# Performance work log

Measured on AMD Instinct MI355X. Metric: run time of the kernel, lower is better.

## Reference

```python
import jax, jax.numpy as jnp
import numpy as np

E, H, D = 512, 8, 64
B, T = 2, 1024
HD = H * D


def _linear(x, W, b):
    return x @ W + b


def _ln(x, g, b):
    mu = x.mean(-1, keepdims=True)
    var = ((x - mu) ** 2).mean(-1, keepdims=True)
    return (x - mu) / jnp.sqrt(var + 1e-5) * g + b


def _l2norm(x):
    n = jnp.sqrt((x * x).sum(-1, keepdims=True))
    return x / jnp.maximum(n, 1e-12)


def setup_inputs() -> dict:
    key = jax.random.key(0)
    ks = jax.random.split(key, 32)
    s = 0.02
    inp = {
        'x': jax.random.normal(ks[0], (B, T, E), jnp.float32),
        'b_min': jax.random.normal(ks[1], (B, T, E), jnp.float32),
        'b_max': jax.random.normal(ks[2], (B, T, E), jnp.float32),
        'motif_context': jax.random.normal(ks[3], (B, T, E), jnp.float32),
        'Wk': jax.random.normal(ks[4], (E, HD), jnp.float32) * s,
        'bk': jnp.zeros((HD,), jnp.float32),
        'Wq': jax.random.normal(ks[5], (E, HD), jnp.float32) * s,
        'bq': jnp.zeros((HD,), jnp.float32),
        'Wv': jax.random.normal(ks[6], (E, HD), jnp.float32) * s,
        'bv': jnp.zeros((HD,), jnp.float32),
        'Wo': jax.random.normal(ks[7], (HD, E), jnp.float32) * s,
        'bo': jnp.zeros((E,), jnp.float32),
        'Wd': jax.random.normal(ks[8], (E, H), jnp.float32) * s,
        'bd': jnp.zeros((H,), jnp.float32),
        'Wgw': jax.random.normal(ks[9], (E, H), jnp.float32) * s,
        'bgw': jnp.zeros((H,), jnp.float32),
        'Wgf': jax.random.normal(ks[10], (E, H), jnp.float32) * s,
        'bgf': jnp.zeros((H,), jnp.float32),
        'Wps': jax.random.normal(ks[11], (E, E), jnp.float32) * s,
        'bps': jnp.zeros((E,), jnp.float32),
        'ln1_g': jnp.ones((E,), jnp.float32),
        'ln1_b': jnp.zeros((E,), jnp.float32),
        'ln2_g': jnp.ones((E,), jnp.float32),
        'ln2_b': jnp.zeros((E,), jnp.float32),
        'W1': jax.random.normal(ks[12], (E, 4 * E), jnp.float32) * s,
        'b1': jnp.zeros((4 * E,), jnp.float32),
        'W2': jax.random.normal(ks[13], (4 * E, E), jnp.float32) * s,
        'b2': jnp.zeros((E,), jnp.float32),
    }
    return inp


def reference(x, b_min, b_max, motif_context,
              Wk, bk, Wq, bq, Wv, bv, Wo, bo, Wd, bd,
              Wgw, bgw, Wgf, bgf, Wps, bps,
              ln1_g, ln1_b, ln2_g, ln2_b, W1, b1, W2, b2):
    Bs, Ts, Es = x.shape
    x_n = _ln(x, ln1_g, ln1_b)
    k = _l2norm(_linear(x_n, Wk, bk).reshape(Bs, Ts, H, D))
    q = _l2norm(_linear(x_n, Wq, bq).reshape(Bs, Ts, H, D))
    v = jnp.tanh(_linear(x_n, Wv, bv).reshape(Bs, Ts, H, D))
    d = jax.nn.softplus(_linear(x_n, Wd, bd))            # (B,T,H)
    gw = jax.nn.sigmoid(_linear(x_n, Wgw, bgw)) ** 2     # (B,T,H)
    gf = 1.0 - jax.nn.sigmoid(_linear(x_n, Wgf, bgf)) ** 2

    # gated linear recurrent scan via cumsum of rank-1 updates
    v_gated = v * (d * gw)[..., None]                    # (B,T,H,D)
    updates = jnp.einsum('bthi,bthj->bthij', v_gated, k)  # (B,T,H,D,D)
    decay = jnp.clip(d * gf, 1e-6, 0.999)
    log_decay = jnp.log(decay)[..., None, None]          # (B,T,H,1,1)
    exp_cum_decay = jnp.exp(jnp.cumsum(log_decay, axis=1))
    state = jnp.cumsum(updates / (exp_cum_decay + 1e-8), axis=1) * exp_cum_decay
    readout = jnp.einsum('bthij,bthj->bthi', state, q)   # (B,T,H,D)
    next_mem = state[:, -1]

    x2 = x + _linear(readout.reshape(Bs, Ts, HD), Wo, bo) + 0.1 * motif_context
    h = _ln(x2, ln2_g, ln2_b)
    x3 = x2 + _linear(jax.nn.gelu(_linear(h, W1, b1), approximate=False), W2, b2)
    probe = _linear(x3, Wps, bps)
    return (x3, next_mem, b_min + probe, b_max + probe)
```

## Files before the change

### kernel.cpp

```cpp
#include <hip/hip_runtime.h>


typedef unsigned short u16;
typedef unsigned int u32;
typedef __attribute__((ext_vector_type(8))) short short8;
typedef __attribute__((ext_vector_type(4))) float floatx4;

__device__ __forceinline__ float b2f(u16 u) {
  u32 x = ((u32)u) << 16;
  return __uint_as_float(x);
}
__device__ __forceinline__ u16 f2b(float f) {
  u32 x = __float_as_uint(f);
  u32 r = (x + 0x7fffu + ((x >> 16) & 1u)) >> 16;
  return (u16)r;
}
__device__ __forceinline__ float4 b4_to_f4(uint2 u) {
  float4 r;
  r.x = __uint_as_float((u.x & 0xffffu) << 16);
  r.y = __uint_as_float(u.x & 0xffff0000u);
  r.z = __uint_as_float((u.y & 0xffffu) << 16);
  r.w = __uint_as_float(u.y & 0xffff0000u);
  return r;
}

__device__ __forceinline__ void stage16(const u16* g, u16* lds_wave_base) {
  __builtin_amdgcn_global_load_lds((const __attribute__((address_space(1))) void*)g,
                                   (__attribute__((address_space(3))) void*)lds_wave_base,
                                   16, 0, 0);
}

template <int ROWS>
__device__ __forceinline__ void stage_tile64(const u16* __restrict__ G, int ldK, int kb,
                                             u16* lds, int tid) {
#pragma unroll
  for (int r = 0; r < ROWS / 32; ++r) {
    int slot = r * 256 + tid;
    int row = slot >> 3;
    int kwg = (slot & 7) ^ (row & 7);
    stage16(G + (size_t)row * ldK + kb * 64 + kwg * 8,
            lds + (size_t)(r * 256 + (tid >> 6) * 64) * 8);
  }
}

__device__ __forceinline__ void ln_row(const float* __restrict__ xr,
                                       const float* __restrict__ g,
                                       const float* __restrict__ bt,
                                       u16* __restrict__ yr, int tid, float* red) {
  float x0 = xr[tid], x1 = xr[tid + 256];
  float s = x0 + x1, ss = x0 * x0 + x1 * x1;
#pragma unroll
  for (int o = 32; o > 0; o >>= 1) { s += __shfl_xor(s, o); ss += __shfl_xor(ss, o); }
  if ((tid & 63) == 0) { red[tid >> 6] = s; red[4 + (tid >> 6)] = ss; }
  __syncthreads();
  float ts = red[0] + red[1] + red[2] + red[3];
  float tss = red[4] + red[5] + red[6] + red[7];
  float mu = ts * (1.f / 512.f);
  float var = tss * (1.f / 512.f) - mu * mu;
  float rstd = 1.0f / sqrtf(var + 1e-5f);
  yr[tid] = f2b((x0 - mu) * rstd * g[tid] + bt[tid]);
  yr[tid + 256] = f2b((x1 - mu) * rstd * g[tid + 256] + bt[tid + 256]);
}

__global__ __launch_bounds__(256) void prep_weights(
    const float* __restrict__ Wk, const float* __restrict__ Wq,
    const float* __restrict__ Wv, const float* __restrict__ Wo,
    const float* __restrict__ Wps, const float* __restrict__ W1,
    const float* __restrict__ W2, const float* __restrict__ Wd,
    const float* __restrict__ Wgw, const float* __restrict__ Wgf,
    const float* __restrict__ bk, const float* __restrict__ bq,
    const float* __restrict__ bv, const float* __restrict__ bd,
    const float* __restrict__ bgw, const float* __restrict__ bgf,
    const float* __restrict__ x, const float* __restrict__ ln1g,
    const float* __restrict__ ln1b,
    u16* __restrict__ WTQ, u16* __restrict__ WTO, u16* __restrict__ WTPS,
    u16* __restrict__ WT1, u16* __restrict__ WT2, float* __restrict__ BQV,
    u16* __restrict__ XN) {
  int bid = blockIdx.x, tid = threadIdx.x;
  __shared__ float tile[32][33];
  __shared__ float red[8];
  if (bid < 3328) {
    const float* src;
    u16* dst;
    int C, rel, tiles_x;
    if (bid < 256)       { src = Wk;  dst = WTQ;           C = 512;  rel = bid;        tiles_x = 16; }
    else if (bid < 512)  { src = Wq;  dst = WTQ + 262144;  C = 512;  rel = bid - 256;  tiles_x = 16; }
    else if (bid < 768)  { src = Wv;  dst = WTQ + 524288;  C = 512;  rel = bid - 512;  tiles_x = 16; }
    else if (bid < 1024) { src = Wo;  dst = WTO;           C = 512;  rel = bid - 768;  tiles_x = 16; }
    else if (bid < 1280) { src = Wps; dst = WTPS;          C = 512;  rel = bid - 1024; tiles_x = 16; }
    else if (bid < 2304) { src = W1;  dst = WT1;           C = 2048; rel = bid - 1280; tiles_x = 64; }
    else                 { src = W2;  dst = WT2;           C = 512;  rel = bid - 2304; tiles_x = 16; }
    int R = (bid >= 1280 && bid < 2304) ? 512 : (bid >= 2304 ? 2048 : 512);
    int c0 = (rel % tiles_x) * 32, r0 = (rel / tiles_x) * 32;
    int tx = tid & 31, ty = tid >> 5;
#pragma unroll
    for (int i = 0; i < 4; ++i)
      tile[ty + i * 8][tx] = src[(size_t)(r0 + ty + i * 8) * C + c0 + tx];
    __syncthreads();
#pragma unroll
    for (int i = 0; i < 4; ++i)
      dst[(size_t)(c0 + ty + i * 8) * R + r0 + tx] = f2b(tile[tx][ty + i * 8]);
  } else if (bid < 3392) {
    int idx = (bid - 3328) * 256 + tid;
    const int stride = 64 * 256;
    for (int i = idx; i < 128 * 512; i += stride) {
      int local = i >> 9, k = i & 511;
      float v = 0.f;
      if (local < 8) v = Wd[k * 8 + local];
      else if (local < 16) v = Wgw[k * 8 + (local - 8)];
      else if (local < 24) v = Wgf[k * 8 + (local - 16)];
      WTQ[(size_t)(1536 + local) * 512 + k] = f2b(v);
    }
    for (int i = idx; i < 1664; i += stride) {
      float v = 0.f;
      if (i < 512) v = bk[i];
      else if (i < 1024) v = bq[i - 512];
      else if (i < 1536) v = bv[i - 1024];
      else if (i < 1544) v = bd[i - 1536];
      else if (i < 1552) v = bgw[i - 1544];
      else if (i < 1560) v = bgf[i - 1552];
      BQV[i] = v;
    }
  } else {
    int row = bid - 3392;
    ln_row(x + (size_t)row * 512, ln1g, ln1b, XN + (size_t)row * 512, tid, red);
  }
}

__global__ __launch_bounds__(256) void ln_f32(const float* __restrict__ X,
                                              const float* __restrict__ g,
                                              const float* __restrict__ bt,
                                              u16* __restrict__ Y) {
  __shared__ float red[8];
  ln_row(X + (size_t)blockIdx.x * 512, g, bt, Y + (size_t)blockIdx.x * 512,
         threadIdx.x, red);
}

template <int BM, int EPI>
__global__ __launch_bounds__(256, (BM == 64 ? 4 : 6)) void gemm2s(
    const u16* __restrict__ A, const u16* __restrict__ BT, const float* __restrict__ bias,
    float* __restrict__ outf, float* __restrict__ outf2, u16* __restrict__ outb,
    const float* __restrict__ aux0, const float* __restrict__ aux1, int M, int N, int K) {
  constexpr int MT = BM / 32;
  constexpr int S = BM / 32 + 2;
  __shared__ __align__(16) u16 As[2][BM * 64];
  __shared__ __align__(16) u16 Bs[2][64 * 64];
  const int tid = threadIdx.x;
  const int lane = tid & 63, wave = tid >> 6;
  const int wm = wave >> 1, wn = wave & 1;
  const int m0 = blockIdx.y * BM, n0 = blockIdx.x * 64;
  floatx4 acc[MT][2] = {};
  const int fr = lane & 15, kq = lane >> 4;
  const int nk = K >> 6;
  const u16* Ab = A + (size_t)m0 * K;
  const u16* Bb = BT + (size_t)n0 * K;

  stage_tile64<BM>(Ab, K, 0, As[0], tid);
  stage_tile64<64>(Bb, K, 0, Bs[0], tid);

  for (int kb = 0; kb < nk; ++kb) {
    const int cur = kb & 1;
    if (kb + 1 < nk) {
      stage_tile64<BM>(Ab, K, kb + 1, As[cur ^ 1], tid);
      stage_tile64<64>(Bb, K, kb + 1, Bs[cur ^ 1], tid);
      if constexpr (S == 4) asm volatile("s_waitcnt vmcnt(4)" ::: "memory");
      else asm volatile("s_waitcnt vmcnt(3)" ::: "memory");
    } else {
      asm volatile("s_waitcnt vmcnt(0)" ::: "memory");
    }
    asm volatile("s_barrier" ::: "memory");

#pragma unroll
    for (int sub = 0; sub < 2; ++sub) {
      short8 af[MT], bf[2];
#pragma unroll
      for (int mt = 0; mt < MT; ++mt) {
        int row = wm * (BM / 2) + mt * 16 + fr;
        int c = sub * 4 + kq;
        af[mt] = *(const short8*)&As[cur][row * 64 + ((c ^ (row & 7)) << 3)];
      }
#pragma unroll
      for (int nt = 0; nt < 2; ++nt) {
        int row = wn * 32 + nt * 16 + fr;
        int c = sub * 4 + kq;
        bf[nt] = *(const short8*)&Bs[cur][row * 64 + ((c ^ (row & 7)) << 3)];
      }
#pragma unroll
      for (int mt = 0; mt < MT; ++mt)
#pragma unroll
        for (int nt = 0; nt < 2; ++nt)
          acc[mt][nt] =
              __builtin_amdgcn_mfma_f32_16x16x32_bf16(af[mt], bf[nt], acc[mt][nt], 0, 0, 0);
    }
    asm volatile("s_waitcnt lgkmcnt(0)" ::: "memory");
    asm volatile("s_barrier" ::: "memory");
  }

  const int col = lane & 15;
  const int rbase = (lane >> 4) * 4;
#pragma unroll
  for (int nt = 0; nt < 2; ++nt) {
    int gc = n0 + wn * 32 + nt * 16 + col;
    float bvv = bias[gc];
#pragma unroll
    for (int mt = 0; mt < MT; ++mt) {
      int gr = m0 + wm * (BM / 2) + mt * 16 + rbase;
#pragma unroll
      for (int r = 0; r < 4; ++r) {
        size_t idx = (size_t)(gr + r) * N + gc;
        float v = acc[mt][nt][r] + bvv;
        if constexpr (EPI == 0) {
          outf[idx] = v;
        } else if constexpr (EPI == 1) {
          outf[idx] = aux0[idx] + v + 0.1f * aux1[idx];
        } else if constexpr (EPI == 2) {
          outb[idx] = f2b(0.5f * v * (1.f + erff(v * 0.70710678118654752f)));
        } else if constexpr (EPI == 3) {
          float w = aux0[idx] + v;
          outf[idx] = w;
          outb[idx] = f2b(w);
        } else {
          outf[idx] = aux0[idx] + v;
          outf2[idx] = aux1[idx] + v;
        }
      }
    }
  }
}

__global__ __launch_bounds__(512) void post_qkvg(const float* __restrict__ C0,
                                                 u16* __restrict__ KB, u16* __restrict__ QB,
                                                 u16* __restrict__ VG,
                                                 float* __restrict__ DEC) {
  int tok = blockIdx.x;
  int b = tok >> 10, t = tok & 1023;
  int tid = threadIdx.x;
  int h = tid >> 6, d = tid & 63;
  const float* row = C0 + (size_t)tok * 1664;

  float dl = row[1536 + h], gwl = row[1544 + h], gfl = row[1552 + h];
  float dd = dl > 20.f ? dl : log1pf(expf(dl));
  float sw = 1.f / (1.f + expf(-gwl));
  float gw = sw * sw;
  float sf = 1.f / (1.f + expf(-gfl));
  float gf = 1.f - sf * sf;

  size_t obase = ((size_t)(b * 8 + h) * 1024 + t) * 64 + d;

  float kx = row[h * 64 + d];
  float ssk = kx * kx;
#pragma unroll
  for (int o = 32; o > 0; o >>= 1) ssk += __shfl_xor(ssk, o);
  KB[obase] = f2b(kx / fmaxf(sqrtf(ssk), 1e-12f));

  float qx = row[512 + h * 64 + d];
  float ssq = qx * qx;
#pragma unroll
  for (int o = 32; o > 0; o >>= 1) ssq += __shfl_xor(ssq, o);
  QB[obase] = f2b(qx / fmaxf(sqrtf(ssq), 1e-12f));

  float vx = tanhf(row[1024 + h * 64 + d]);
  VG[obase] = f2b(vx * (dd * gw));

  if (d == 0)
    DEC[(size_t)(b * 8 + h) * 1024 + t] = fminf(fmaxf(dd * gf, 1e-6f), 0.999f);
}

__global__ void logcum(const float* __restrict__ DEC, float* __restrict__ LC,
                       float* __restrict__ WW) {
  int bh = blockIdx.x;
  int lane = threadIdx.x;
  size_t base = (size_t)bh * 1024 + lane * 16;
  float loc[16];
  float run = 0.f;
#pragma unroll
  for (int i = 0; i < 16; ++i) { run += logf(DEC[base + i]); loc[i] = run; }
  float x = run;
#pragma unroll
  for (int o = 1; o < 64; o <<= 1) {
    float v = __shfl_up(x, o);
    if (lane >= o) x += v;
  }
  float excl = x - run;
#pragma unroll
  for (int i = 0; i < 16; ++i) {
    float L = excl + loc[i];
    LC[base + i] = L;
    float c = expf(L);
    WW[base + i] = c / (c + 1e-8f);
  }
}

__global__ __launch_bounds__(256, 2) void scan_phase1(
    const u16* __restrict__ KB, const u16* __restrict__ QB, const u16* __restrict__ VG,
    const float* __restrict__ DEC, const float* __restrict__ WW,
    float* __restrict__ RP, float* __restrict__ SF) {
  int chunk = blockIdx.x, h = blockIdx.y, b = blockIdx.z;
  int bh = b * 8 + h;
  int t0 = chunk * 32;
  __shared__ __align__(16) float sk[2048], sq[2048], sv[2048];
  __shared__ float lsa[32], lsw[32];
  int tid = threadIdx.x;

  const u16* gk = KB + ((size_t)bh * 1024 + t0) * 64;
  const u16* gq = QB + ((size_t)bh * 1024 + t0) * 64;
  const u16* gv = VG + ((size_t)bh * 1024 + t0) * 64;
#pragma unroll
  for (int r = 0; r < 2; ++r) {
    int f = (r * 256 + tid) * 4;
    *(float4*)&sk[f] = b4_to_f4(*(const uint2*)(gk + f));
    *(float4*)&sq[f] = b4_to_f4(*(const uint2*)(gq + f));
    *(float4*)&sv[f] = b4_to_f4(*(const uint2*)(gv + f));
  }
  if (tid < 32) {
    lsa[tid] = DEC[(size_t)bh * 1024 + t0 + tid];
    lsw[tid] = WW[(size_t)bh * 1024 + t0 + tid];
  }
  __syncthreads();

  int i = tid >> 2, j0 = (tid & 3) * 16;
  float s[16];
#pragma unroll
  for (int z = 0; z < 16; ++z) s[z] = 0.f;

  for (int t = 0; t < 32; ++t) {
    float a = lsa[t], w = lsw[t];
    float wv = w * sv[t * 64 + i];
    float r = 0.f;
#pragma unroll
    for (int u4 = 0; u4 < 4; ++u4) {
      float4 kv = *(const float4*)&sk[t * 64 + j0 + u4 * 4];
      float4 qv = *(const float4*)&sq[t * 64 + j0 + u4 * 4];
      s[u4 * 4 + 0] = fmaf(a, s[u4 * 4 + 0], wv * kv.x); r = fmaf(s[u4 * 4 + 0], qv.x, r);
      s[u4 * 4 + 1] = fmaf(a, s[u4 * 4 + 1], wv * kv.y); r = fmaf(s[u4 * 4 + 1], qv.y, r);
      s[u4 * 4 + 2] = fmaf(a, s[u4 * 4 + 2], wv * kv.z); r = fmaf(s[u4 * 4 + 2], qv.z, r);
      s[u4 * 4 + 3] = fmaf(a, s[u4 * 4 + 3], wv * kv.w); r = fmaf(s[u4 * 4 + 3], qv.w, r);
    }
    r += __shfl_xor(r, 1);
    r += __shfl_xor(r, 2);
    if ((tid & 3) == 0)
      RP[((size_t)(b * 1024 + t0 + t) * 8 + h) * 64 + i] = r;
  }

  float* Sf = SF + ((size_t)bh * 32 + chunk) * 4096 + i * 64 + j0;
#pragma unroll
  for (int u4 = 0; u4 < 4; ++u4) {
    float4 v;
    v.x = s[u4 * 4 + 0]; v.y = s[u4 * 4 + 1]; v.z = s[u4 * 4 + 2]; v.w = s[u4 * 4 + 3];
    *(float4*)&Sf[u4 * 4] = v;
  }
}

__global__ __launch_bounds__(256) void scan_phase2p(const float* __restrict__ SF,
                                                    const float* __restrict__ LC,
                                                    float* __restrict__ SI,
                                                    float* __restrict__ next_mem) {
  int bh = blockIdx.x >> 4;
  int e = (blockIdx.x & 15) * 256 + threadIdx.x;
  float s = 0.f;
  for (int c = 0; c < 32; ++c) {
    SI[((size_t)bh * 32 + c) * 4096 + e] = s;
    float Lend = LC[(size_t)bh * 1024 + c * 32 + 31];
    float Lpre = c ? LC[(size_t)bh * 1024 + c * 32 - 1] : 0.f;
    float P = expf(Lend - Lpre);
    s = fmaf(P, s, SF[((size_t)bh * 32 + c) * 4096 + e]);
  }
  next_mem[(size_t)bh * 4096 + e] = s;
}

__global__ __launch_bounds__(256, 2) void scan_phase3(
    const u16* __restrict__ QB, const float* __restrict__ SI, const float* __restrict__ LC,
    const float* __restrict__ RP, u16* __restrict__ AB) {
  int chunk = blockIdx.x, h = blockIdx.y, b = blockIdx.z;
  int bh = b * 8 + h;
  int t0 = chunk * 32;
  __shared__ __align__(16) float sq[2048];
  __shared__ float sL[32];
  int tid = threadIdx.x;

  const u16* gq = QB + ((size_t)bh * 1024 + t0) * 64;
#pragma unroll
  for (int r = 0; r < 2; ++r) {
    int f = (r * 256 + tid) * 4;
    *(float4*)&sq[f] = b4_to_f4(*(const uint2*)(gq + f));
  }
  if (tid < 32) sL[tid] = LC[(size_t)bh * 1024 + t0 + tid];
  __syncthreads();

  float Lpre = chunk ? LC[(size_t)bh * 1024 + t0 - 1] : 0.f;
  int i = tid >> 2, j0 = (tid & 3) * 16;
  const float* Si = SI + ((size_t)bh * 32 + chunk) * 4096 + i * 64 + j0;
  float S[16];
#pragma unroll
  for (int u4 = 0; u4 < 4; ++u4) {
    float4 v = *(const float4*)&Si[u4 * 4];
    S[u4 * 4 + 0] = v.x; S[u4 * 4 + 1] = v.y; S[u4 * 4 + 2] = v.z; S[u4 * 4 + 3] = v.w;
  }

  for (int t = 0; t < 32; ++t) {
    float p = expf(sL[t] - Lpre);
    float r = 0.f;
#pragma unroll
    for (int u4 = 0; u4 < 4; ++u4) {
      float4 qv = *(const float4*)&sq[t * 64 + j0 + u4 * 4];
      r = fmaf(S[u4 * 4 + 0], qv.x, r);
      r = fmaf(S[u4 * 4 + 1], qv.y, r);
      r = fmaf(S[u4 * 4 + 2], qv.z, r);
      r = fmaf(S[u4 * 4 + 3], qv.w, r);
    }
    r += __shfl_xor(r, 1);
    r += __shfl_xor(r, 2);
    if ((tid & 3) == 0) {
      size_t gi = ((size_t)(b * 1024 + t0 + t) * 8 + h) * 64 + i;
      AB[gi] = f2b(RP[gi] + p * r);
    }
  }
}

extern "C" void kernel_launch(void* const* d_in, const int* in_sizes, int n_in,
                              void* d_out, int out_size, void* d_ws, size_t ws_size,
                              hipStream_t stream) {
  const float* x = (const float*)d_in[0];
  const float* bmin = (const float*)d_in[1];
  const float* bmax = (const float*)d_in[2];
  const float* motif = (const float*)d_in[3];
  const float* Wk = (const float*)d_in[4];
  const float* bk = (const float*)d_in[5];
  const float* Wq = (const float*)d_in[6];
  const float* bq = (const float*)d_in[7];
  const float* Wv = (const float*)d_in[8];
  const float* bv = (const float*)d_in[9];
  const float* Wo = (const float*)d_in[10];
  const float* bo = (const float*)d_in[11];
  const float* Wd = (const float*)d_in[12];
  const float* bd = (const float*)d_in[13];
  const float* Wgw = (const float*)d_in[14];
  const float* bgw = (const float*)d_in[15];
  const float* Wgf = (const float*)d_in[16];
  const float* bgf = (const float*)d_in[17];
  const float* Wps = (const float*)d_in[18];
  const float* bps = (const float*)d_in[19];
  const float* ln1g = (const float*)d_in[20];
  const float* ln1b = (const float*)d_in[21];
  const float* ln2g = (const float*)d_in[22];
  const float* ln2b = (const float*)d_in[23];
  const float* W1 = (const float*)d_in[24];
  const float* b1 = (const float*)d_in[25];
  const float* W2 = (const float*)d_in[26];
  const float* b2 = (const float*)d_in[27];

  char* ws = (char*)d_ws;
  u16* WTQ = (u16*)(ws + 0);
  u16* WTO = (u16*)(ws + 1703936);
  u16* WT1 = (u16*)(ws + 2228224);
  u16* WT2 = (u16*)(ws + 4325376);
  u16* WTPS = (u16*)(ws + 6422528);
  float* BQV = (float*)(ws + 6946816);
  u16* XN = (u16*)(ws + 6953984);
  float* C0 = (float*)(ws + 9051136);
  u16* KB = (u16*)(ws + 22682624);
  u16* QB = (u16*)(ws + 24779776);
  u16* VG = (u16*)(ws + 26876928);
  float* DEC = (float*)(ws + 28974080);
  float* LC = (float*)(ws + 29039616);
  float* WW = (float*)(ws + 29105152);
  float* RP = (float*)(ws + 29170688);
  float* SF = (float*)(ws + 33364992);
  float* SI = (float*)(ws + 41753600);
  u16* AB = (u16*)(ws + 9051136);
  float* X2 = (float*)(ws + 11148288);
  u16* HB = (u16*)(ws + 15342592);
  u16* MID = (u16*)(ws + 17439744);
  u16* X3B = (u16*)(ws + 26876928);

  float* out0 = (float*)d_out;
  float* out1 = out0 + 1048576;
  float* out2 = out0 + 1114112;
  float* out3 = out0 + 2162688;

  prep_weights<<<5440, 256, 0, stream>>>(Wk, Wq, Wv, Wo, Wps, W1, W2, Wd, Wgw, Wgf,
                                         bk, bq, bv, bd, bgw, bgf, x, ln1g, ln1b,
                                         WTQ, WTO, WTPS, WT1, WT2, BQV, XN);
  gemm2s<64, 0><<<dim3(26, 32), 256, 0, stream>>>(XN, WTQ, BQV, C0, nullptr, nullptr,
                                                  nullptr, nullptr, 2048, 1664, 512);
  post_qkvg<<<2048, 512, 0, stream>>>(C0, KB, QB, VG, DEC);
  logcum<<<16, 64, 0, stream>>>(DEC, LC, WW);
  scan_phase1<<<dim3(32, 8, 2), 256, 0, stream>>>(KB, QB, VG, DEC, WW, RP, SF);
  scan_phase2p<<<256, 256, 0, stream>>>(SF, LC, SI, out1);
  scan_phase3<<<dim3(32, 8, 2), 256, 0, stream>>>(QB, SI, LC, RP, AB);

  gemm2s<32, 1><<<dim3(8, 64), 256, 0, stream>>>(AB, WTO, bo, X2, nullptr, nullptr,
                                                 x, motif, 2048, 512, 512);
  ln_f32<<<2048, 256, 0, stream>>>(X2, ln2g, ln2b, HB);
  gemm2s<64, 2><<<dim3(32, 32), 256, 0, stream>>>(HB, WT1, b1, nullptr, nullptr, MID,
                                                  nullptr, nullptr, 2048, 2048, 512);
  gemm2s<32, 3><<<dim3(8, 64), 256, 0, stream>>>(MID, WT2, b2, out0, nullptr, X3B,
                                                 X2, nullptr, 2048, 512, 2048);
  gemm2s<32, 4><<<dim3(8, 64), 256, 0, stream>>>(X3B, WTPS, bps, out2, out3, nullptr,
                                                 bmin, bmax, 2048, 512, 512);
}
```

Baseline: 234.7 us.

## Fuse QKV post-processing into GEMM epilogue and merge gate computation with log-cumsum

```diff
diff --git a/kernel.cpp b/kernel.cpp
--- a/kernel.cpp
+++ b/kernel.cpp
@@ -140,11 +140,13 @@
 __global__ __launch_bounds__(256, (BM == 64 ? 4 : 6)) void gemm2s(
     const u16* __restrict__ A, const u16* __restrict__ BT, const float* __restrict__ bias,
     float* __restrict__ outf, float* __restrict__ outf2, u16* __restrict__ outb,
+    u16* __restrict__ outb2, u16* __restrict__ outb3,
     const float* __restrict__ aux0, const float* __restrict__ aux1, int M, int N, int K) {
   constexpr int MT = BM / 32;
   constexpr int S = BM / 32 + 2;
   __shared__ __align__(16) u16 As[2][BM * 64];
   __shared__ __align__(16) u16 Bs[2][64 * 64];
+  __shared__ float ssb[2][BM];
   const int tid = threadIdx.x;
   const int lane = tid & 63, wave = tid >> 6;
   const int wm = wave >> 1, wn = wave & 1;
@@ -198,103 +200,164 @@
 
   const int col = lane & 15;
   const int rbase = (lane >> 4) * 4;
+
+  float vv[MT][2][4];
 #pragma unroll
   for (int nt = 0; nt < 2; ++nt) {
     int gc = n0 + wn * 32 + nt * 16 + col;
     float bvv = bias[gc];
 #pragma unroll
-    for (int mt = 0; mt < MT; ++mt) {
-      int gr = m0 + wm * (BM / 2) + mt * 16 + rbase;
-#pragma unroll
-      for (int r = 0; r < 4; ++r) {
-        size_t idx = (size_t)(gr + r) * N + gc;
-        float v = acc[mt][nt][r] + bvv;
-        if constexpr (EPI == 0) {
-          outf[idx] = v;
-        } else if constexpr (EPI == 1) {
-          outf[idx] = aux0[idx] + v + 0.1f * aux1[idx];
-        } else if constexpr (EPI == 2) {
-          outb[idx] = f2b(0.5f * v * (1.f + erff(v * 0.70710678118654752f)));
-        } else if constexpr (EPI == 3) {
-          float w = aux0[idx] + v;
-          outf[idx] = w;
-          outb[idx] = f2b(w);
-        } else {
-          outf[idx] = aux0[idx] + v;
-          outf2[idx] = aux1[idx] + v;
+    for (int mt = 0; mt < MT; ++mt)
+#pragma unroll
+      for (int r = 0; r < 4; ++r) vv[mt][nt][r] = acc[mt][nt][r] + bvv;
+  }
+
+  if constexpr (EPI == 5) {
+    const int sec = n0 >> 9;
+    const int h = (n0 & 511) >> 6;
+    if (sec == 3) {
+#pragma unroll
+      for (int nt = 0; nt < 2; ++nt) {
+        int gcl = (n0 - 1536) + wn * 32 + nt * 16 + col;
+#pragma unroll
+        for (int mt = 0; mt < MT; ++mt) {
+          int gr = m0 + wm * (BM / 2) + mt * 16 + rbase;
+#pragma unroll
+          for (int r = 0; r < 4; ++r)
+            outf[(size_t)(gr + r) * 128 + gcl] = vv[mt][nt][r];
         }
       }
-    }
-  }
-}
-
-__global__ __launch_bounds__(512) void post_qkvg(const float* __restrict__ C0,
-                                                 u16* __restrict__ KB, u16* __restrict__ QB,
-                                                 u16* __restrict__ VG,
-                                                 float* __restrict__ DEC) {
-  int tok = blockIdx.x;
-  int b = tok >> 10, t = tok & 1023;
+    } else if (sec == 2) {
+#pragma unroll
+      for (int nt = 0; nt < 2; ++nt) {
+        int d = wn * 32 + nt * 16 + col;
+#pragma unroll
+        for (int mt = 0; mt < MT; ++mt) {
+          int gr = m0 + wm * (BM / 2) + mt * 16 + rbase;
+#pragma unroll
+          for (int r = 0; r < 4; ++r) {
+            int tok = gr + r;
+            int bh = (tok >> 10) * 8 + h;
+            outb3[((size_t)bh * 1024 + (tok & 1023)) * 64 + d] = f2b(tanhf(vv[mt][nt][r]));
+          }
+        }
+      }
+    } else {
+#pragma unroll
+      for (int mt = 0; mt < MT; ++mt) {
+#pragma unroll
+        for (int r = 0; r < 4; ++r) {
+          float ss = vv[mt][0][r] * vv[mt][0][r] + vv[mt][1][r] * vv[mt][1][r];
+          ss += __shfl_xor(ss, 1);
+          ss += __shfl_xor(ss, 2);
+          ss += __shfl_xor(ss, 4);
+          ss += __shfl_xor(ss, 8);
+          if ((lane & 15) == 0)
+            ssb[wn][wm * (BM / 2) + mt * 16 + rbase + r] = ss;
+        }
+      }
+      __syncthreads();
+      u16* dst = (sec == 0) ? outb : outb2;
+#pragma unroll
+      for (int mt = 0; mt < MT; ++mt) {
+#pragma unroll
+        for (int r = 0; r < 4; ++r) {
+          int br = wm * (BM / 2) + mt * 16 + rbase + r;
+          float tot = ssb[0][br] + ssb[1][br];
+          float rs = 1.0f / fmaxf(sqrtf(tot), 1e-12f);
+          int tok = m0 + br;
+          int bh = (tok >> 10) * 8 + h;
+          size_t base = ((size_t)bh * 1024 + (tok & 1023)) * 64;
+#pragma unroll
+          for (int nt = 0; nt < 2; ++nt) {
+            int d = wn * 32 + nt * 16 + col;
+            dst[base + d] = f2b(vv[mt][nt][r] * rs);
+          }
+        }
+      }
+    }
+  } else {
+#pragma unroll
+    for (int nt = 0; nt < 2; ++nt) {
+      int gc = n0 + wn * 32 + nt * 16 + col;
+#pragma unroll
+      for (int mt = 0; mt < MT; ++mt) {
+        int gr = m0 + wm * (BM / 2) + mt * 16 + rbase;
+#pragma unroll
+        for (int r = 0; r < 4; ++r) {
+          size_t idx = (size_t)(gr + r) * N + gc;
+          float v = vv[mt][nt][r];
+          if constexpr (EPI == 1) {
+            outf[idx] = aux0[idx] + v + 0.1f * aux1[idx];
+          } else if constexpr (EPI == 2) {
+            outb[idx] = f2b(0.5f * v * (1.f + erff(v * 0.70710678118654752f)));
+          } else if constexpr (EPI == 3) {
+            float w = aux0[idx] + v;
+            outf[idx] = w;
+            outb[idx] = f2b(w);
+          } else if constexpr (EPI == 4) {
+            outf[idx] = aux0[idx] + v;
+            outf2[idx] = aux1[idx] + v;
+          }
+        }
+      }
+    }
+  }
+}
+
+__global__ __launch_bounds__(256) void gates_logcum(
+    const float* __restrict__ G0, float* __restrict__ DEC, float* __restrict__ SVG,
+    float* __restrict__ LC, float* __restrict__ WW) {
+  int bh = blockIdx.x;
+  int b = bh >> 3, h = bh & 7;
   int tid = threadIdx.x;
-  int h = tid >> 6, d = tid & 63;
-  const float* row = C0 + (size_t)tok * 1664;
-
-  float dl = row[1536 + h], gwl = row[1544 + h], gfl = row[1552 + h];
-  float dd = dl > 20.f ? dl : log1pf(expf(dl));
-  float sw = 1.f / (1.f + expf(-gwl));
-  float gw = sw * sw;
-  float sf = 1.f / (1.f + expf(-gfl));
-  float gf = 1.f - sf * sf;
-
-  size_t obase = ((size_t)(b * 8 + h) * 1024 + t) * 64 + d;
-
-  float kx = row[h * 64 + d];
-  float ssk = kx * kx;
-#pragma unroll
-  for (int o = 32; o > 0; o >>= 1) ssk += __shfl_xor(ssk, o);
-  KB[obase] = f2b(kx / fmaxf(sqrtf(ssk), 1e-12f));
-
-  float qx = row[512 + h * 64 + d];
-  float ssq = qx * qx;
-#pragma unroll
-  for (int o = 32; o > 0; o >>= 1) ssq += __shfl_xor(ssq, o);
-  QB[obase] = f2b(qx / fmaxf(sqrtf(ssq), 1e-12f));
-
-  float vx = tanhf(row[1024 + h * 64 + d]);
-  VG[obase] = f2b(vx * (dd * gw));
-
-  if (d == 0)
-    DEC[(size_t)(b * 8 + h) * 1024 + t] = fminf(fmaxf(dd * gf, 1e-6f), 0.999f);
-}
-
-__global__ void logcum(const float* __restrict__ DEC, float* __restrict__ LC,
-                       float* __restrict__ WW) {
-  int bh = blockIdx.x;
-  int lane = threadIdx.x;
-  size_t base = (size_t)bh * 1024 + lane * 16;
-  float loc[16];
-  float run = 0.f;
-#pragma unroll
-  for (int i = 0; i < 16; ++i) { run += logf(DEC[base + i]); loc[i] = run; }
-  float x = run;
-#pragma unroll
-  for (int o = 1; o < 64; o <<= 1) {
-    float v = __shfl_up(x, o);
-    if (lane >= o) x += v;
-  }
-  float excl = x - run;
-#pragma unroll
-  for (int i = 0; i < 16; ++i) {
-    float L = excl + loc[i];
-    LC[base + i] = L;
-    float c = expf(L);
-    WW[base + i] = c / (c + 1e-8f);
+  __shared__ float ldec[1024];
+#pragma unroll
+  for (int tt = 0; tt < 4; ++tt) {
+    int t = tt * 256 + tid;
+    size_t tok = (size_t)b * 1024 + t;
+    float dl = G0[tok * 128 + h];
+    float gwl = G0[tok * 128 + 8 + h];
+    float gfl = G0[tok * 128 + 16 + h];
+    float dd = dl > 20.f ? dl : log1pf(expf(dl));
+    float sw = 1.f / (1.f + expf(-gwl));
+    float gw = sw * sw;
+    float sf = 1.f / (1.f + expf(-gfl));
+    float gf = 1.f - sf * sf;
+    float dec = fminf(fmaxf(dd * gf, 1e-6f), 0.999f);
+    ldec[t] = dec;
+    DEC[(size_t)bh * 1024 + t] = dec;
+    SVG[(size_t)bh * 1024 + t] = dd * gw;
+  }
+  __syncthreads();
+  if (tid < 64) {
+    int lane = tid;
+    size_t base = (size_t)bh * 1024 + lane * 16;
+    float loc[16];
+    float run = 0.f;
+#pragma unroll
+    for (int i = 0; i < 16; ++i) { run += logf(ldec[lane * 16 + i]); loc[i] = run; }
+    float x = run;
+#pragma unroll
+    for (int o = 1; o < 64; o <<= 1) {
+      float v = __shfl_up(x, o);
+      if (lane >= o) x += v;
+    }
+    float excl = x - run;
+#pragma unroll
+    for (int i = 0; i < 16; ++i) {
+      float L = excl + loc[i];
+      LC[base + i] = L;
+      float c = expf(L);
+      WW[base + i] = c / (c + 1e-8f);
+    }
   }
 }
 
 __global__ __launch_bounds__(256, 2) void scan_phase1(
-    const u16* __restrict__ KB, const u16* __restrict__ QB, const u16* __restrict__ VG,
+    const u16* __restrict__ KB, const u16* __restrict__ QB, const u16* __restrict__ VB,
     const float* __restrict__ DEC, const float* __restrict__ WW,
-    float* __restrict__ RP, float* __restrict__ SF) {
+    const float* __restrict__ SVG, float* __restrict__ RP, float* __restrict__ SF) {
   int chunk = blockIdx.x, h = blockIdx.y, b = blockIdx.z;
   int bh = b * 8 + h;
   int t0 = chunk * 32;
@@ -304,7 +367,7 @@
 
   const u16* gk = KB + ((size_t)bh * 1024 + t0) * 64;
   const u16* gq = QB + ((size_t)bh * 1024 + t0) * 64;
-  const u16* gv = VG + ((size_t)bh * 1024 + t0) * 64;
+  const u16* gv = VB + ((size_t)bh * 1024 + t0) * 64;
 #pragma unroll
   for (int r = 0; r < 2; ++r) {
     int f = (r * 256 + tid) * 4;
@@ -313,8 +376,9 @@
     *(float4*)&sv[f] = b4_to_f4(*(const uint2*)(gv + f));
   }
   if (tid < 32) {
-    lsa[tid] = DEC[(size_t)bh * 1024 + t0 + tid];
-    lsw[tid] = WW[(size_t)bh * 1024 + t0 + tid];
+    size_t gi = (size_t)bh * 1024 + t0 + tid;
+    lsa[tid] = DEC[gi];
+    lsw[tid] = WW[gi] * SVG[gi];
   }
   __syncthreads();
 
@@ -457,21 +521,22 @@
   u16* WTPS = (u16*)(ws + 6422528);
   float* BQV = (float*)(ws + 6946816);
   u16* XN = (u16*)(ws + 6953984);
-  float* C0 = (float*)(ws + 9051136);
-  u16* KB = (u16*)(ws + 22682624);
-  u16* QB = (u16*)(ws + 24779776);
-  u16* VG = (u16*)(ws + 26876928);
-  float* DEC = (float*)(ws + 28974080);
-  float* LC = (float*)(ws + 29039616);
-  float* WW = (float*)(ws + 29105152);
-  float* RP = (float*)(ws + 29170688);
-  float* SF = (float*)(ws + 33364992);
-  float* SI = (float*)(ws + 41753600);
-  u16* AB = (u16*)(ws + 9051136);
-  float* X2 = (float*)(ws + 11148288);
-  u16* HB = (u16*)(ws + 15342592);
-  u16* MID = (u16*)(ws + 17439744);
-  u16* X3B = (u16*)(ws + 26876928);
+  float* G0 = (float*)(ws + 9051136);
+  u16* KB = (u16*)(ws + 10099712);
+  u16* QB = (u16*)(ws + 12196864);
+  u16* VB = (u16*)(ws + 14294016);
+  float* DEC = (float*)(ws + 16391168);
+  float* LC = (float*)(ws + 16456704);
+  float* WW = (float*)(ws + 16522240);
+  float* SVG = (float*)(ws + 16587776);
+  float* RP = (float*)(ws + 16653312);
+  float* SF = (float*)(ws + 20847616);
+  float* SI = (float*)(ws + 29236224);
+  u16* AB = (u16*)(ws + 37624832);
+  float* X2 = (float*)(ws + 39721984);
+  u16* HB = (u16*)(ws + 43916288);
+  u16* MID = (u16*)(ws + 9051136);
+  u16* X3B = (u16*)(ws + 20847616);
 
   float* out0 = (float*)d_out;
   float* out1 = out0 + 1048576;
@@ -481,21 +546,23 @@
   prep_weights<<<5440, 256, 0, stream>>>(Wk, Wq, Wv, Wo, Wps, W1, W2, Wd, Wgw, Wgf,
                                          bk, bq, bv, bd, bgw, bgf, x, ln1g, ln1b,
                                          WTQ, WTO, WTPS, WT1, WT2, BQV, XN);
-  gemm2s<64, 0><<<dim3(26, 32), 256, 0, stream>>>(XN, WTQ, BQV, C0, nullptr, nullptr,
+  gemm2s<64, 5><<<dim3(26, 32), 256, 0, stream>>>(XN, WTQ, BQV, G0, nullptr, KB, QB, VB,
                                                   nullptr, nullptr, 2048, 1664, 512);
-  post_qkvg<<<2048, 512, 0, stream>>>(C0, KB, QB, VG, DEC);
-  logcum<<<16, 64, 0, stream>>>(DEC, LC, WW);
-  scan_phase1<<<dim3(32, 8, 2), 256, 0, stream>>>(KB, QB, VG, DEC, WW, RP, SF);
+  gates_logcum<<<16, 256, 0, stream>>>(G0, DEC, SVG, LC, WW);
+  scan_phase1<<<dim3(32, 8, 2), 256, 0, stream>>>(KB, QB, VB, DEC, WW, SVG, RP, SF);
   scan_phase2p<<<256, 256, 0, stream>>>(SF, LC, SI, out1);
   scan_phase3<<<dim3(32, 8, 2), 256, 0, stream>>>(QB, SI, LC, RP, AB);
 
   gemm2s<32, 1><<<dim3(8, 64), 256, 0, stream>>>(AB, WTO, bo, X2, nullptr, nullptr,
-                                                 x, motif, 2048, 512, 512);
+                                                 nullptr, nullptr, x, motif, 2048, 512, 512);
   ln_f32<<<2048, 256, 0, stream>>>(X2, ln2g, ln2b, HB);
   gemm2s<64, 2><<<dim3(32, 32), 256, 0, stream>>>(HB, WT1, b1, nullptr, nullptr, MID,
-                                                  nullptr, nullptr, 2048, 2048, 512);
+                                                  nullptr, nullptr, nullptr, nullptr,
+                                                  2048, 2048, 512);
   gemm2s<32, 3><<<dim3(8, 64), 256, 0, stream>>>(MID, WT2, b2, out0, nullptr, X3B,
-                                                 X2, nullptr, 2048, 512, 2048);
+                                                 nullptr, nullptr, X2, nullptr,
+                                                 2048, 512, 2048);
   gemm2s<32, 4><<<dim3(8, 64), 256, 0, stream>>>(X3B, WTPS, bps, out2, out3, nullptr,
-                                                 bmin, bmax, 2048, 512, 512);
-}
+                                                 nullptr, nullptr, bmin, bmax,
+                                                 2048, 512, 512);
+}
```

New measurement: 230.3 us. No clear change (-1.9%).
